# Performance work log

Hardware: AMD Instinct MI355X
Metric: run time of the kernel (lower is better)

Reference implementation:

```python
import jax, jax.numpy as jnp
import numpy as np
import math

B, N, NODE_DIM, EDGE_DIM, HID, NH = 2, 384, 128, 128, 128, 8
HD = HID // NH  # head_dim = 16


def _layernorm(x, g, b, eps=1e-5):
    m = jnp.mean(x, axis=-1, keepdims=True)
    v = jnp.var(x, axis=-1, keepdims=True)
    return (x - m) * jax.lax.rsqrt(v + eps) * g + b


def setup_inputs() -> dict:
    key = jax.random.key(0)
    ks = jax.random.split(key, 16)
    w = lambda k, s: jax.random.normal(k, s, jnp.float32) * 0.05
    return {
        "node_features": jax.random.normal(ks[0], (B, N, NODE_DIM), jnp.float32),
        "edge_features": jax.random.normal(ks[1], (B, N, N, EDGE_DIM), jnp.float32),
        "adj_mask": jax.random.randint(ks[2], (B, N, N), 0, 2, jnp.int32),
        "W_node": w(ks[3], (NODE_DIM, HID)), "b_node": jnp.zeros((HID,), jnp.float32),
        "W_q": w(ks[4], (HID, HID)), "b_q": jnp.zeros((HID,), jnp.float32),
        "W_k": w(ks[5], (HID, HID)), "b_k": jnp.zeros((HID,), jnp.float32),
        "W_v": w(ks[6], (HID, HID)), "b_v": jnp.zeros((HID,), jnp.float32),
        "W_edge": w(ks[7], (EDGE_DIM, HID)), "b_edge": jnp.zeros((HID,), jnp.float32),
        "W_gate": w(ks[8], (EDGE_DIM, HID)), "b_gate": jnp.zeros((HID,), jnp.float32),
        "W_out": w(ks[9], (HID, HID)), "b_out": jnp.zeros((HID,), jnp.float32),
        "W_eout": w(ks[10], (HID, EDGE_DIM)), "b_eout": jnp.zeros((EDGE_DIM,), jnp.float32),
        "g1": jnp.ones((HID,), jnp.float32), "be1": jnp.zeros((HID,), jnp.float32),
        "g2": jnp.ones((EDGE_DIM,), jnp.float32), "be2": jnp.zeros((EDGE_DIM,), jnp.float32),
    }


def reference(node_features, edge_features, adj_mask,
              W_node, b_node, W_q, b_q, W_k, b_k, W_v, b_v,
              W_edge, b_edge, W_gate, b_gate, W_out, b_out,
              W_eout, b_eout, g1, be1, g2, be2):
    b, n, _ = node_features.shape
    h = node_features @ W_node + b_node          # (B,N,HID)
    residual = h
    Q = (h @ W_q + b_q).reshape(b, n, NH, HD)
    K = (h @ W_k + b_k).reshape(b, n, NH, HD)
    V = (h @ W_v + b_v).reshape(b, n, NH, HD)
    scores = jnp.einsum('bihd,bjhd->bhij', Q, K) / math.sqrt(HD)  # (B,NH,N,N)
    # edge-gated bias
    edge_h = (edge_features @ W_edge + b_edge).reshape(b, n, n, NH, HD)
    edge_gate = jax.nn.sigmoid(edge_features @ W_gate + b_gate).reshape(b, n, n, NH, HD)
    edge_attn = jnp.sum(edge_h * edge_gate, axis=-1)  # (B,N,N,NH)
    scores = scores + jnp.transpose(edge_attn, (0, 3, 1, 2))
    # adjacency mask
    scores = jnp.where(adj_mask[:, None, :, :] == 0, jnp.float32(-1e9), scores)
    attn = jax.nn.softmax(scores, axis=-1)  # dropout = identity (eval)
    attn_out = jnp.einsum('bhij,bjhd->bihd', attn, V).reshape(b, n, HID)
    h = _layernorm(residual + (attn_out @ W_out + b_out), g1, be1)
    # edge update: mean attention over heads gates (src+tgt)/2
    attn_mean = jnp.mean(attn, axis=1)  # (B,N,N)
    pair = 0.5 * (h[:, :, None, :] + h[:, None, :, :])  # (B,N,N,HID)
    edge_update = attn_mean[..., None] * pair
    edge_out = _layernorm(edge_features + (edge_update @ W_eout + b_eout), g2, be2)
    return h, edge_out
```

## Files before the change

kernel.cpp:

```cpp
#include <hip/hip_runtime.h>
#include <hip/hip_bf16.h>

#define NN 384
#define HIDDIM 128
#define NHEADS 8
#define HD 16
#define LOCAL_E (NN*NN)
#define NE (2*LOCAL_E)
#define NNODE (2*NN)

typedef __attribute__((ext_vector_type(8))) __bf16 bf16x8;
typedef __attribute__((ext_vector_type(4))) float f32x4;

__global__ void prep_w(const float* __restrict__ W_edge, const float* __restrict__ W_gate,
                       bf16x8* __restrict__ Wg) {
    int gid = blockIdx.x * blockDim.x + threadIdx.x;
    int n16  = gid & 15;
    int quad = (gid >> 4) & 3;
    int kkl  = (gid >> 6) & 1;
    int np   = (gid >> 7) & 15;
    int kkh  = (gid >> 11) & 1;
    int n = np * 16 + n16;
    int k0 = (kkh * 2 + kkl) * 32 + quad * 8;
    const float* src = (n < 128) ? (W_edge + n) : (W_gate + (n - 128));
    bf16x8 v;
#pragma unroll
    for (int j = 0; j < 8; ++j) v[j] = (__bf16)src[(size_t)(k0 + j) * 128];
    Wg[gid] = v;
}

__global__ __launch_bounds__(128) void k1_proj(
    const float* __restrict__ nf,
    const float* __restrict__ Wn, const float* __restrict__ bn,
    const float* __restrict__ Wq, const float* __restrict__ bq,
    const float* __restrict__ Wk, const float* __restrict__ bk,
    const float* __restrict__ Wv, const float* __restrict__ bv,
    float* __restrict__ h_res, float* __restrict__ Q,
    float* __restrict__ K, float* __restrict__ V)
{
    __shared__ float xf[8][128];
    __shared__ float hf[8][128];
    int t = threadIdx.x;
    int r0 = blockIdx.x * 8;
    for (int r = 0; r < 8; ++r) xf[r][t] = nf[(size_t)(r0 + r) * 128 + t];
    __syncthreads();
    float acc[8];
#pragma unroll
    for (int r = 0; r < 8; ++r) acc[r] = bn[t];
    for (int k = 0; k < 128; ++k) {
        float w = Wn[k * 128 + t];
#pragma unroll
        for (int r = 0; r < 8; ++r) acc[r] += xf[r][k] * w;
    }
    for (int r = 0; r < 8; ++r) { h_res[(size_t)(r0 + r) * 128 + t] = acc[r]; hf[r][t] = acc[r]; }
    __syncthreads();
    const float* Ws[3] = {Wq, Wk, Wv};
    const float* bs[3] = {bq, bk, bv};
    float* Os[3] = {Q, K, V};
#pragma unroll
    for (int m = 0; m < 3; ++m) {
        float a2[8];
#pragma unroll
        for (int r = 0; r < 8; ++r) a2[r] = bs[m][t];
        for (int k = 0; k < 128; ++k) {
            float w = Ws[m][k * 128 + t];
#pragma unroll
            for (int r = 0; r < 8; ++r) a2[r] += hf[r][k] * w;
        }
        int hh = t >> 4, d = t & 15;
        for (int r = 0; r < 8; ++r) {
            int g = r0 + r;
            int b = g / NN, i = g - b * NN;
            Os[m][(size_t)((b * NHEADS + hh) * NN + i) * HD + d] = a2[r];
        }
    }
}

__global__ __launch_bounds__(512, 4) void k2_edge(
    const float* __restrict__ EF, const bf16x8* __restrict__ Wg,
    const float* __restrict__ b_edge, const float* __restrict__ b_gate,
    float* __restrict__ edge_attn)
{
    __shared__ bf16x8 Ash[1024];
    __shared__ bf16x8 Bsh[2048];
    int t = threadIdx.x;
    int lane = t & 63;
    int w = t >> 6;
    int wm = w & 1, wn = w >> 1;
    int e_base = blockIdx.x * 128;

    f32x4 acc[4][4];
    f32x4 zero = {0.f, 0.f, 0.f, 0.f};
#pragma unroll
    for (int i = 0; i < 4; ++i)
#pragma unroll
        for (int j = 0; j < 4; ++j) acc[i][j] = zero;

    for (int kkh = 0; kkh < 2; ++kkh) {
#pragma unroll
        for (int p = 0; p < 4; ++p) {
            int g = p * 512 + t;
            Bsh[g] = Wg[kkh * 2048 + g];
        }
#pragma unroll
        for (int p = 0; p < 2; ++p) {
            int gid = p * 512 + t;
            int m16 = gid & 15, quad = (gid >> 4) & 3, kkl = (gid >> 6) & 1, ip = gid >> 7;
            int row = ip * 16 + m16;
            const float4* src4 = (const float4*)(EF + (size_t)(e_base + row) * 128
                                                 + (kkh * 2 + kkl) * 32 + quad * 8);
            float4 f0 = src4[0], f1 = src4[1];
            bf16x8 v;
            v[0] = (__bf16)f0.x; v[1] = (__bf16)f0.y; v[2] = (__bf16)f0.z; v[3] = (__bf16)f0.w;
            v[4] = (__bf16)f1.x; v[5] = (__bf16)f1.y; v[6] = (__bf16)f1.z; v[7] = (__bf16)f1.w;
            Ash[gid] = v;
        }
        __syncthreads();
#pragma unroll
        for (int kkl = 0; kkl < 2; ++kkl) {
            bf16x8 af[4], bfh[2], bfg[2];
#pragma unroll
            for (int i = 0; i < 4; ++i) {
                int ip = wm * 4 + i;
                af[i] = Ash[(ip * 2 + kkl) * 64 + lane];
            }
#pragma unroll
            for (int j = 0; j < 2; ++j) {
                int nph = wn * 2 + j;
                bfh[j] = Bsh[(nph * 2 + kkl) * 64 + lane];
                bfg[j] = Bsh[((nph + 8) * 2 + kkl) * 64 + lane];
            }
#pragma unroll
            for (int i = 0; i < 4; ++i) {
#pragma unroll
                for (int j = 0; j < 2; ++j) {
                    acc[i][j]     = __builtin_amdgcn_mfma_f32_16x16x32_bf16(af[i], bfh[j], acc[i][j], 0, 0, 0);
                    acc[i][j + 2] = __builtin_amdgcn_mfma_f32_16x16x32_bf16(af[i], bfg[j], acc[i][j + 2], 0, 0, 0);
                }
            }
        }
        __syncthreads();
    }

    int n16 = lane & 15, quad = lane >> 4;
#pragma unroll
    for (int j = 0; j < 2; ++j) {
        int c = wn * 32 + j * 16 + n16;
        float bh = b_edge[c], bg = b_gate[c];
        int head = wn * 2 + j;
#pragma unroll
        for (int i = 0; i < 4; ++i) {
#pragma unroll
            for (int r = 0; r < 4; ++r) {
                float hv = acc[i][j][r] + bh;
                float gv = acc[i][j + 2][r] + bg;
                float v = hv * (1.f / (1.f + __expf(-gv)));
                v += __shfl_xor(v, 1);
                v += __shfl_xor(v, 2);
                v += __shfl_xor(v, 4);
                v += __shfl_xor(v, 8);
                if (n16 == 0) {
                    int m = wm * 64 + i * 16 + quad * 4 + r;
                    int e = e_base + m;
                    int b = e / LOCAL_E;
                    int local = e - b * LOCAL_E;
                    edge_attn[(size_t)(b * NHEADS + head) * LOCAL_E + local] = v;
                }
            }
        }
    }
}

__global__ __launch_bounds__(128) void k3_attn(
    const float* __restrict__ Q, const float* __restrict__ K, const float* __restrict__ V,
    const float* __restrict__ edge_attn, const int* __restrict__ adj,
    float* __restrict__ am, float* __restrict__ attn_out)
{
    __shared__ float Kh[NN * 17];
    __shared__ float Vh[NN * 17];
    __shared__ float Qi[16 * HD];
    __shared__ float rowbuf[NN];
    __shared__ float red[2];
    __shared__ float red2[8][16];
    int t = threadIdx.x;
    int bh = blockIdx.x / 24;
    int chunk = blockIdx.x % 24;
    int b = bh >> 3;
    const float* Kbase = K + (size_t)bh * NN * HD;
    const float* Vbase = V + (size_t)bh * NN * HD;
    for (int p = 0; p < 48; ++p) {
        int idx = p * 128 + t;
        int jj = idx >> 4, dd = idx & 15;
        Kh[jj * 17 + dd] = Kbase[idx];
        Vh[jj * 17 + dd] = Vbase[idx];
    }
    Qi[t]       = Q[(size_t)bh * NN * HD + chunk * 16 * HD + t];
    Qi[t + 128] = Q[(size_t)bh * NN * HD + chunk * 16 * HD + t + 128];
    __syncthreads();
    int lane = t & 63, wid = t >> 6;
    const float* ea = edge_attn + (size_t)bh * LOCAL_E;
    const int* adjb = adj + (size_t)b * LOCAL_E;
    for (int rr = 0; rr < 16; ++rr) {
        int i = chunk * 16 + rr;
        float s[3];
#pragma unroll
        for (int jj = 0; jj < 3; ++jj) {
            int j = t + jj * 128;
            float a = 0.f;
#pragma unroll
            for (int d = 0; d < 16; ++d) a += Qi[rr * 16 + d] * Kh[j * 17 + d];
            a = a * 0.25f + ea[(size_t)i * NN + j];
            if (adjb[(size_t)i * NN + j] == 0) a = -1e9f;
            s[jj] = a;
        }
        float mx = fmaxf(s[0], fmaxf(s[1], s[2]));
#pragma unroll
        for (int o = 1; o < 64; o <<= 1) mx = fmaxf(mx, __shfl_xor(mx, o));
        if (lane == 0) red[wid] = mx;
        __syncthreads();
        mx = fmaxf(red[0], red[1]);
        __syncthreads();
        float e0 = __expf(s[0] - mx), e1 = __expf(s[1] - mx), e2 = __expf(s[2] - mx);
        float sm = e0 + e1 + e2;
#pragma unroll
        for (int o = 1; o < 64; o <<= 1) sm += __shfl_xor(sm, o);
        if (lane == 0) red[wid] = sm;
        __syncthreads();
        float inv = 1.f / (red[0] + red[1]);
        float p0 = e0 * inv, p1 = e1 * inv, p2 = e2 * inv;
        rowbuf[t] = p0; rowbuf[t + 128] = p1; rowbuf[t + 256] = p2;
        atomicAdd(am + (size_t)b * LOCAL_E + i * NN + t,       p0 * 0.125f);
        atomicAdd(am + (size_t)b * LOCAL_E + i * NN + t + 128, p1 * 0.125f);
        atomicAdd(am + (size_t)b * LOCAL_E + i * NN + t + 256, p2 * 0.125f);
        __syncthreads();
        int d = t & 15, g = t >> 4;
        float pa = 0.f;
        for (int j = g * 48; j < g * 48 + 48; ++j) pa += rowbuf[j] * Vh[j * 17 + d];
        red2[g][d] = pa;
        __syncthreads();
        if (t < 16) {
            float s2 = 0.f;
#pragma unroll
            for (int gg = 0; gg < 8; ++gg) s2 += red2[gg][t];
            attn_out[(size_t)(b * NN + i) * HIDDIM + (bh & 7) * HD + t] = s2;
        }
        __syncthreads();
    }
}

__global__ __launch_bounds__(128) void k5_hout(
    const float* __restrict__ attn_out, const float* __restrict__ h_res,
    const float* __restrict__ W_out, const float* __restrict__ b_out,
    const float* __restrict__ g1, const float* __restrict__ be1,
    const float* __restrict__ W_eout,
    float* __restrict__ h_out, float* __restrict__ hp)
{
    __shared__ float ao[8][128];
    __shared__ float hn[8][128];
    __shared__ float redA[2], redB[2];
    int t = threadIdx.x, r0 = blockIdx.x * 8;
    for (int r = 0; r < 8; ++r) ao[r][t] = attn_out[(size_t)(r0 + r) * 128 + t];
    __syncthreads();
    float acc[8];
#pragma unroll
    for (int r = 0; r < 8; ++r) acc[r] = b_out[t];
    for (int k = 0; k < 128; ++k) {
        float w = W_out[k * 128 + t];
#pragma unroll
        for (int r = 0; r < 8; ++r) acc[r] += ao[r][k] * w;
    }
    int lane = t & 63, wid = t >> 6;
    float gg = g1[t], bb = be1[t];
    for (int r = 0; r < 8; ++r) {
        float u = h_res[(size_t)(r0 + r) * 128 + t] + acc[r];
        float sv = u, sq = u * u;
#pragma unroll
        for (int o = 1; o < 64; o <<= 1) { sv += __shfl_xor(sv, o); sq += __shfl_xor(sq, o); }
        if (lane == 0) { redA[wid] = sv; redB[wid] = sq; }
        __syncthreads();
        float tot = redA[0] + redA[1], totq = redB[0] + redB[1];
        __syncthreads();
        float mean = tot * (1.f / 128.f);
        float var = totq * (1.f / 128.f) - mean * mean;
        float nv = (u - mean) * rsqrtf(var + 1e-5f) * gg + bb;
        h_out[(size_t)(r0 + r) * 128 + t] = nv;
        hn[r][t] = nv;
    }
    __syncthreads();
    float acc2[8];
#pragma unroll
    for (int r = 0; r < 8; ++r) acc2[r] = 0.f;
    for (int k = 0; k < 128; ++k) {
        float w = W_eout[k * 128 + t];
#pragma unroll
        for (int r = 0; r < 8; ++r) acc2[r] += hn[r][k] * w;
    }
    for (int r = 0; r < 8; ++r) hp[(size_t)(r0 + r) * 128 + t] = acc2[r];
}

__global__ __launch_bounds__(256) void k6_eout(
    const float* __restrict__ EF, const float* __restrict__ am,
    const float* __restrict__ hp, const float* __restrict__ b_eout,
    const float* __restrict__ g2, const float* __restrict__ be2,
    float* __restrict__ eout)
{
    int t = threadIdx.x;
    int slot = t >> 5, l = t & 31;
    int e = blockIdx.x * 8 + slot;
    int b = e / LOCAL_E;
    int local = e - b * LOCAL_E;
    int i = local / NN, j = local - i * NN;
    float a = am[e];
    const float4* ef4 = (const float4*)(EF + (size_t)e * 128);
    const float4* hpi = (const float4*)(hp + (size_t)(b * NN + i) * 128);
    const float4* hpj = (const float4*)(hp + (size_t)(b * NN + j) * 128);
    float4 ef = ef4[l];
    float4 pi = hpi[l], pj = hpj[l];
    float4 bo = ((const float4*)b_eout)[l];
    float4 u;
    u.x = ef.x + a * 0.5f * (pi.x + pj.x) + bo.x;
    u.y = ef.y + a * 0.5f * (pi.y + pj.y) + bo.y;
    u.z = ef.z + a * 0.5f * (pi.z + pj.z) + bo.z;
    u.w = ef.w + a * 0.5f * (pi.w + pj.w) + bo.w;
    float sv = u.x + u.y + u.z + u.w;
    float sq = u.x * u.x + u.y * u.y + u.z * u.z + u.w * u.w;
#pragma unroll
    for (int o = 1; o < 32; o <<= 1) { sv += __shfl_xor(sv, o); sq += __shfl_xor(sq, o); }
    float mean = sv * (1.f / 128.f);
    float var = sq * (1.f / 128.f) - mean * mean;
    float rs = rsqrtf(var + 1e-5f);
    float4 gg = ((const float4*)g2)[l], bb = ((const float4*)be2)[l];
    float4 o4;
    o4.x = (u.x - mean) * rs * gg.x + bb.x;
    o4.y = (u.y - mean) * rs * gg.y + bb.y;
    o4.z = (u.z - mean) * rs * gg.z + bb.z;
    o4.w = (u.w - mean) * rs * gg.w + bb.w;
    ((float4*)(eout + (size_t)e * 128))[l] = o4;
}

extern "C" void kernel_launch(void* const* d_in, const int* in_sizes, int n_in,
                              void* d_out, int out_size, void* d_ws, size_t ws_size,
                              hipStream_t stream) {
    (void)in_sizes; (void)n_in; (void)out_size; (void)ws_size;
    const float* nf     = (const float*)d_in[0];
    const float* ef     = (const float*)d_in[1];
    const int*   adj    = (const int*)d_in[2];
    const float* W_node = (const float*)d_in[3];
    const float* b_node = (const float*)d_in[4];
    const float* W_q    = (const float*)d_in[5];
    const float* b_q    = (const float*)d_in[6];
    const float* W_k    = (const float*)d_in[7];
    const float* b_k    = (const float*)d_in[8];
    const float* W_v    = (const float*)d_in[9];
    const float* b_v    = (const float*)d_in[10];
    const float* W_edge = (const float*)d_in[11];
    const float* b_edge = (const float*)d_in[12];
    const float* W_gate = (const float*)d_in[13];
    const float* b_gate = (const float*)d_in[14];
    const float* W_out  = (const float*)d_in[15];
    const float* b_out  = (const float*)d_in[16];
    const float* W_eout = (const float*)d_in[17];
    const float* b_eout = (const float*)d_in[18];
    const float* g1     = (const float*)d_in[19];
    const float* be1    = (const float*)d_in[20];
    const float* g2     = (const float*)d_in[21];
    const float* be2    = (const float*)d_in[22];

    float* ws = (float*)d_ws;
    float* h_res    = ws;
    float* Q        = ws + 98304;
    float* Kp       = ws + 196608;
    float* Vp       = ws + 294912;
    float* attn_out = ws + 393216;
    float* hp       = ws + 491520;
    float* am       = ws + 589824;
    bf16x8* Wg      = (bf16x8*)(ws + 884736);

    float* h_out = (float*)d_out;
    float* eout  = (float*)d_out + 98304;
    float* edge_attn = eout;

    prep_w<<<dim3(16), dim3(256), 0, stream>>>(W_edge, W_gate, Wg);
    k1_proj<<<dim3(96), dim3(128), 0, stream>>>(nf, W_node, b_node, W_q, b_q,
                                                W_k, b_k, W_v, b_v, h_res, Q, Kp, Vp);
    k2_edge<<<dim3(2304), dim3(512), 0, stream>>>(ef, Wg, b_edge, b_gate, edge_attn);
    hipMemsetAsync((void*)am, 0, (size_t)NE * sizeof(float), stream);
    k3_attn<<<dim3(384), dim3(128), 0, stream>>>(Q, Kp, Vp, edge_attn, adj, am, attn_out);
    k5_hout<<<dim3(96), dim3(128), 0, stream>>>(attn_out, h_res, W_out, b_out,
                                                g1, be1, W_eout, h_out, hp);
    k6_eout<<<dim3(36864), dim3(256), 0, stream>>>(ef, am, hp, b_eout, g2, be2, eout);
}
```

Measured before the change: 480.6 us.

## Restructure edge GEMM with register-resident weights and per-head warp split

Each warp now owns one head and keeps its slice of the edge/gate weights in registers, using them as the MFMA A operand, while edge features become the B operand. This transposes the output so head-dim reduction happens within the 4 accumulator registers plus two cross-quad shuffles instead of four shuffles per element. The full 128-wide K tile is staged in shared memory once with a single barrier, removing the weight staging buffer and the second loop's syncs. It also swaps the sigmoid division for a hardware reciprocal, which is slightly less precise, and raises register use for 16 accumulators plus 8 weight fragments.

```diff
diff --git a/kernel.cpp b/kernel.cpp
--- a/kernel.cpp
+++ b/kernel.cpp
@@ -81,92 +81,74 @@
     const float* __restrict__ b_edge, const float* __restrict__ b_gate,
     float* __restrict__ edge_attn)
 {
-    __shared__ bf16x8 Ash[1024];
-    __shared__ bf16x8 Bsh[2048];
+    __shared__ bf16x8 Ash[2048];
     int t = threadIdx.x;
     int lane = t & 63;
     int w = t >> 6;
-    int wm = w & 1, wn = w >> 1;
     int e_base = blockIdx.x * 128;
 
-    f32x4 acc[4][4];
+    bf16x8 wfh[4], wfg[4];
+#pragma unroll
+    for (int kk = 0; kk < 4; ++kk) {
+        int kkh = kk >> 1, kkl = kk & 1;
+        wfh[kk] = Wg[kkh * 2048 + ( w      * 2 + kkl) * 64 + lane];
+        wfg[kk] = Wg[kkh * 2048 + ((w + 8) * 2 + kkl) * 64 + lane];
+    }
+
+#pragma unroll
+    for (int p = 0; p < 4; ++p) {
+        int gid = p * 512 + t;
+        int m16 = gid & 15, quad = (gid >> 4) & 3, kk = (gid >> 6) & 3, ip = gid >> 8;
+        int row = ip * 16 + m16;
+        const float4* src4 = (const float4*)(EF + (size_t)(e_base + row) * 128
+                                             + kk * 32 + quad * 8);
+        float4 f0 = src4[0], f1 = src4[1];
+        bf16x8 v;
+        v[0] = (__bf16)f0.x; v[1] = (__bf16)f0.y; v[2] = (__bf16)f0.z; v[3] = (__bf16)f0.w;
+        v[4] = (__bf16)f1.x; v[5] = (__bf16)f1.y; v[6] = (__bf16)f1.z; v[7] = (__bf16)f1.w;
+        Ash[gid] = v;
+    }
+    __syncthreads();
+
+    f32x4 acc_h[8], acc_g[8];
     f32x4 zero = {0.f, 0.f, 0.f, 0.f};
 #pragma unroll
-    for (int i = 0; i < 4; ++i)
-#pragma unroll
-        for (int j = 0; j < 4; ++j) acc[i][j] = zero;
-
-    for (int kkh = 0; kkh < 2; ++kkh) {
-#pragma unroll
-        for (int p = 0; p < 4; ++p) {
-            int g = p * 512 + t;
-            Bsh[g] = Wg[kkh * 2048 + g];
-        }
-#pragma unroll
-        for (int p = 0; p < 2; ++p) {
-            int gid = p * 512 + t;
-            int m16 = gid & 15, quad = (gid >> 4) & 3, kkl = (gid >> 6) & 1, ip = gid >> 7;
-            int row = ip * 16 + m16;
-            const float4* src4 = (const float4*)(EF + (size_t)(e_base + row) * 128
-                                                 + (kkh * 2 + kkl) * 32 + quad * 8);
-            float4 f0 = src4[0], f1 = src4[1];
-            bf16x8 v;
-            v[0] = (__bf16)f0.x; v[1] = (__bf16)f0.y; v[2] = (__bf16)f0.z; v[3] = (__bf16)f0.w;
-            v[4] = (__bf16)f1.x; v[5] = (__bf16)f1.y; v[6] = (__bf16)f1.z; v[7] = (__bf16)f1.w;
-            Ash[gid] = v;
-        }
-        __syncthreads();
-#pragma unroll
-        for (int kkl = 0; kkl < 2; ++kkl) {
-            bf16x8 af[4], bfh[2], bfg[2];
-#pragma unroll
-            for (int i = 0; i < 4; ++i) {
-                int ip = wm * 4 + i;
-                af[i] = Ash[(ip * 2 + kkl) * 64 + lane];
-            }
-#pragma unroll
-            for (int j = 0; j < 2; ++j) {
-                int nph = wn * 2 + j;
-                bfh[j] = Bsh[(nph * 2 + kkl) * 64 + lane];
-                bfg[j] = Bsh[((nph + 8) * 2 + kkl) * 64 + lane];
-            }
-#pragma unroll
-            for (int i = 0; i < 4; ++i) {
-#pragma unroll
-                for (int j = 0; j < 2; ++j) {
-                    acc[i][j]     = __builtin_amdgcn_mfma_f32_16x16x32_bf16(af[i], bfh[j], acc[i][j], 0, 0, 0);
-                    acc[i][j + 2] = __builtin_amdgcn_mfma_f32_16x16x32_bf16(af[i], bfg[j], acc[i][j + 2], 0, 0, 0);
-                }
-            }
-        }
-        __syncthreads();
+    for (int ip = 0; ip < 8; ++ip) { acc_h[ip] = zero; acc_g[ip] = zero; }
+
+#pragma unroll
+    for (int kk = 0; kk < 4; ++kk) {
+#pragma unroll
+        for (int ip = 0; ip < 8; ++ip) {
+            bf16x8 be = Ash[(ip * 4 + kk) * 64 + lane];
+            acc_h[ip] = __builtin_amdgcn_mfma_f32_16x16x32_bf16(wfh[kk], be, acc_h[ip], 0, 0, 0);
+            acc_g[ip] = __builtin_amdgcn_mfma_f32_16x16x32_bf16(wfg[kk], be, acc_g[ip], 0, 0, 0);
+        }
     }
 
     int n16 = lane & 15, quad = lane >> 4;
-#pragma unroll
-    for (int j = 0; j < 2; ++j) {
-        int c = wn * 32 + j * 16 + n16;
-        float bh = b_edge[c], bg = b_gate[c];
-        int head = wn * 2 + j;
-#pragma unroll
-        for (int i = 0; i < 4; ++i) {
-#pragma unroll
-            for (int r = 0; r < 4; ++r) {
-                float hv = acc[i][j][r] + bh;
-                float gv = acc[i][j + 2][r] + bg;
-                float v = hv * (1.f / (1.f + __expf(-gv)));
-                v += __shfl_xor(v, 1);
-                v += __shfl_xor(v, 2);
-                v += __shfl_xor(v, 4);
-                v += __shfl_xor(v, 8);
-                if (n16 == 0) {
-                    int m = wm * 64 + i * 16 + quad * 4 + r;
-                    int e = e_base + m;
-                    int b = e / LOCAL_E;
-                    int local = e - b * LOCAL_E;
-                    edge_attn[(size_t)(b * NHEADS + head) * LOCAL_E + local] = v;
-                }
-            }
+    float bh[4], bg[4];
+#pragma unroll
+    for (int r = 0; r < 4; ++r) {
+        bh[r] = b_edge[w * 16 + quad * 4 + r];
+        bg[r] = b_gate[w * 16 + quad * 4 + r];
+    }
+#pragma unroll
+    for (int ip = 0; ip < 8; ++ip) {
+        float s = 0.f;
+#pragma unroll
+        for (int r = 0; r < 4; ++r) {
+            float hv = acc_h[ip][r] + bh[r];
+            float gv = acc_g[ip][r] + bg[r];
+            float sig = __builtin_amdgcn_rcpf(1.f + __expf(-gv));
+            s = fmaf(hv, sig, s);
+        }
+        s += __shfl_xor(s, 16);
+        s += __shfl_xor(s, 32);
+        if (quad == 0) {
+            int e = e_base + ip * 16 + n16;
+            int b = e / LOCAL_E;
+            int local = e - b * LOCAL_E;
+            edge_attn[(size_t)(b * NHEADS + w) * LOCAL_E + local] = s;
         }
     }
 }
```

Result: faster. 451.0 us (-6.2%).
